# Optimization experiments

Hardware: AMD Instinct MI355X
Metric: run time of the kernel (lower is better)

## Reference

```python
import jax, jax.numpy as jnp
import numpy as np

D_MODEL, HIDDEN, N_EXPERTS, TOP_K = 1024, 2048, 8, 2
RMS_EPS = 1e-6


def setup_inputs() -> dict:
    key = jax.random.key(0)
    ks = jax.random.split(key, 6)
    B, S = 4, 2048
    return {
        "x": jax.random.normal(ks[0], (B, S, D_MODEL), jnp.float32),
        "norm_weight": jnp.ones((D_MODEL,), jnp.float32),
        "gate_w": jax.random.normal(ks[1], (N_EXPERTS, D_MODEL), jnp.float32) * 0.02,
        "w1": jax.random.normal(ks[2], (N_EXPERTS, HIDDEN, D_MODEL), jnp.float32) * 0.02,
        "b1": jnp.zeros((N_EXPERTS, HIDDEN), jnp.float32),
        "w2": jax.random.normal(ks[3], (N_EXPERTS, D_MODEL, HIDDEN), jnp.float32) * 0.02,
        "b2": jnp.zeros((N_EXPERTS, D_MODEL), jnp.float32),
    }


def reference(x, norm_weight, gate_w, w1, b1, w2, b2):
    B, S, D = x.shape
    E = gate_w.shape[0]
    # RMSNorm
    t = x * jax.lax.rsqrt(jnp.mean(x * x, axis=-1, keepdims=True) + RMS_EPS) * norm_weight
    tokens = t.reshape(-1, D)                      # [T, D]
    T = tokens.shape[0]
    # Top-k routing (eval mode: no gate noise)
    gate_logits = tokens @ gate_w.T                # [T, E]
    gate_scores, expert_idx = jax.lax.top_k(gate_logits, TOP_K)
    routing_weights = jax.nn.softmax(gate_scores, axis=-1)  # [T, K]
    # Per-token per-expert combine weight (scatter routing weights into [T, E])
    combine = jnp.zeros((T, E), tokens.dtype).at[
        jnp.arange(T)[:, None], expert_idx
    ].add(routing_weights)
    # Scan over experts; inactive tokens have combine weight 0, matching the
    # masked gather/scatter-add math of the original exactly.
    def body(acc, params):
        W1, B1, W2, B2, c = params                 # c: [T]
        h = jax.nn.gelu(tokens @ W1.T + B1, approximate=False)  # [T, H]
        o = h @ W2.T + B2                          # [T, D]
        return acc + c[:, None] * o, None

    out, _ = jax.lax.scan(body, jnp.zeros_like(tokens), (w1, b1, w2, b2, combine.T))
    return x + out.reshape(B, S, D)
```

## Files before the change

kernel.cpp:

```cpp
#include <hip/hip_runtime.h>
#include <hip/hip_bf16.h>
#include <stdint.h>

#define D_MODEL 1024
#define HIDDEN  2048
#define N_EXP   8
#define T_TOK   8192
#define MAXPOS  17408
#define ROWTILES (MAXPOS/128)

typedef __attribute__((ext_vector_type(4))) float f32x4;
typedef __attribute__((ext_vector_type(8))) short short8v;

__device__ __forceinline__ unsigned short f2bf(float f) {
    union { float f; unsigned int u; } v; v.f = f;
    unsigned int u = v.u;
    unsigned int r = (u + 0x7fffu + ((u >> 16) & 1u)) >> 16;
    return (unsigned short)r;
}

__device__ __forceinline__ void gload_lds16(const void* g, void* l) {
    __builtin_amdgcn_global_load_lds(
        reinterpret_cast<const __attribute__((address_space(1))) unsigned int*>(
            reinterpret_cast<uintptr_t>(g)),
        reinterpret_cast<__attribute__((address_space(3))) unsigned int*>(
            (uint32_t)reinterpret_cast<uintptr_t>(l)),
        16, 0, 0);
}

__global__ void rms_gate_kernel(const float* __restrict__ x,
                                const float* __restrict__ nw,
                                const float* __restrict__ gw,
                                unsigned short* __restrict__ tb,
                                int* __restrict__ tok_e,
                                float* __restrict__ tok_w) {
    const int wave = threadIdx.x >> 6;
    const int lane = threadIdx.x & 63;
    const int t = blockIdx.x * 4 + wave;

    const float4* xr = (const float4*)(x + (size_t)t * D_MODEL);
    const float4* wr = (const float4*)nw;
    float4 xv[4], wv[4];
    #pragma unroll
    for (int j = 0; j < 4; j++) {
        xv[j] = xr[j * 64 + lane];
        wv[j] = wr[j * 64 + lane];
    }

    float ssq = 0.0f;
    #pragma unroll
    for (int j = 0; j < 4; j++)
        ssq += xv[j].x * xv[j].x + xv[j].y * xv[j].y + xv[j].z * xv[j].z + xv[j].w * xv[j].w;
    #pragma unroll
    for (int off = 32; off; off >>= 1) ssq += __shfl_xor(ssq, off);
    const float scale = rsqrtf(ssq * (1.0f / D_MODEL) + 1e-6f);

    float4 tn[4];
    #pragma unroll
    for (int j = 0; j < 4; j++) {
        tn[j].x = xv[j].x * wv[j].x * scale;
        tn[j].y = xv[j].y * wv[j].y * scale;
        tn[j].z = xv[j].z * wv[j].z * scale;
        tn[j].w = xv[j].w * wv[j].w * scale;
    }

    ushort4* tw = (ushort4*)(tb + (size_t)t * D_MODEL);
    #pragma unroll
    for (int j = 0; j < 4; j++) {
        ushort4 o;
        o.x = f2bf(tn[j].x); o.y = f2bf(tn[j].y);
        o.z = f2bf(tn[j].z); o.w = f2bf(tn[j].w);
        tw[j * 64 + lane] = o;
    }

    float d[8];
    #pragma unroll
    for (int e = 0; e < 8; e++) {
        d[e] = 0.0f;
        #pragma unroll
        for (int j = 0; j < 4; j++) {
            float4 g = ((const float4*)(gw + e * D_MODEL))[j * 64 + lane];
            d[e] += tn[j].x * g.x + tn[j].y * g.y + tn[j].z * g.z + tn[j].w * g.w;
        }
    }
    #pragma unroll
    for (int e = 0; e < 8; e++) {
        #pragma unroll
        for (int off = 32; off; off >>= 1) d[e] += __shfl_xor(d[e], off);
    }

    if (lane == 0) {
        int i0 = 0;
        #pragma unroll
        for (int e = 1; e < 8; e++) if (d[e] > d[i0]) i0 = e;
        int i1 = -1;
        #pragma unroll
        for (int e = 0; e < 8; e++)
            if (e != i0 && (i1 < 0 || d[e] > d[i1])) i1 = e;
        float e1 = expf(d[i1] - d[i0]);
        float w0 = 1.0f / (1.0f + e1);
        ((int2*)tok_e)[t]   = make_int2(i0, i1);
        ((float2*)tok_w)[t] = make_float2(w0, e1 * w0);
    }
}

__global__ void hist_kernel(const int* __restrict__ tok_e, int* __restrict__ counts) {
    __shared__ int lh[8];
    if (threadIdx.x < 8) lh[threadIdx.x] = 0;
    __syncthreads();
    int i = blockIdx.x * 512 + threadIdx.x;
    atomicAdd(&lh[tok_e[i]], 1);
    atomicAdd(&lh[tok_e[i + 256]], 1);
    __syncthreads();
    if (threadIdx.x < 8) atomicAdd(&counts[threadIdx.x], lh[threadIdx.x]);
}

__global__ void scan_fill_kernel(int* __restrict__ perm_tok, float* __restrict__ perm_w,
                                 const int* __restrict__ counts,
                                 int* __restrict__ poff, int* __restrict__ pos_ctr) {
    int i = blockIdx.x * 256 + threadIdx.x;
    if (i < MAXPOS) { perm_tok[i] = 0; perm_w[i] = 0.0f; }
    if (blockIdx.x == 0 && threadIdx.x == 0) {
        int acc = 0; poff[0] = 0;
        #pragma unroll
        for (int e = 0; e < 8; e++) {
            pos_ctr[e] = 0;
            acc += (counts[e] + 127) & ~127;
            poff[e + 1] = acc;
        }
    }
}

__global__ void scatter_kernel(const int* __restrict__ tok_e, const float* __restrict__ tok_w,
                               const int* __restrict__ poff, int* __restrict__ pos_ctr,
                               int* __restrict__ perm_tok, float* __restrict__ perm_w) {
    __shared__ int lh[8], lbase[8];
    if (threadIdx.x < 8) lh[threadIdx.x] = 0;
    __syncthreads();
    int t = blockIdx.x * 256 + threadIdx.x;
    int2   ee = ((const int2*)tok_e)[t];
    float2 ww = ((const float2*)tok_w)[t];
    int p0 = atomicAdd(&lh[ee.x], 1);
    int p1 = atomicAdd(&lh[ee.y], 1);
    __syncthreads();
    if (threadIdx.x < 8) lbase[threadIdx.x] = atomicAdd(&pos_ctr[threadIdx.x], lh[threadIdx.x]);
    __syncthreads();
    int q0 = poff[ee.x] + lbase[ee.x] + p0;
    int q1 = poff[ee.y] + lbase[ee.y] + p1;
    perm_tok[q0] = t; perm_w[q0] = ww.x;
    perm_tok[q1] = t; perm_w[q1] = ww.y;
}

__global__ void cvt_bf16_kernel(const float4* __restrict__ in,
                                ushort4* __restrict__ outp, int n4) {
    int i = blockIdx.x * blockDim.x + threadIdx.x;
    if (i >= n4) return;
    float4 v = in[i];
    ushort4 o; o.x = f2bf(v.x); o.y = f2bf(v.y); o.z = f2bf(v.z); o.w = f2bf(v.w);
    outp[i] = o;
}

template <int MODE, int K, int N>
__global__ void moe_gemm_kernel(const unsigned short* __restrict__ A,
                                const unsigned short* __restrict__ W,
                                const float* __restrict__ bias,
                                const int* __restrict__ perm_tok,
                                const float* __restrict__ perm_w,
                                const int* __restrict__ poff,
                                unsigned short* __restrict__ Hout,
                                float* __restrict__ Out) {
    constexpr int NT = N / 128;
    __shared__ short lds[2 * 128 * 64];
    short* Asm = lds;
    short* Bsm = lds + 128 * 64;

    const int nwg = gridDim.x;
    const int cpx = nwg >> 3;
    const int bid = (int)blockIdx.x;
    const int swz = (bid & 7) * cpx + (bid >> 3);

    const int rt = swz / NT, nt = swz % NT;
    const int row_base = rt * 128;
    if (row_base >= poff[8]) return;
    int e = 0;
    while (poff[e + 1] <= row_base) ++e;
    const int n0 = nt * 128;

    const int tid = threadIdx.x;
    const int wave = tid >> 6, lane = tid & 63;
    const int colb = (tid & 7) * 16;
    const int wr = wave >> 1, wc = wave & 1;

    size_t aoff[4], boff[4];
    #pragma unroll
    for (int i = 0; i < 4; i++) {
        int r = row_base + i * 32 + (tid >> 3);
        int arow = (MODE == 1) ? perm_tok[r] : r;
        aoff[i] = (size_t)arow * (K * 2);
        int brow = n0 + i * 32 + (tid >> 3);
        boff[i] = ((size_t)e * N + brow) * (size_t)(K * 2);
    }
    const char* Ab = (const char*)A;
    const char* Wb = (const char*)W;

    f32x4 acc[4][4];
    #pragma unroll
    for (int mi = 0; mi < 4; mi++)
        #pragma unroll
        for (int ni = 0; ni < 4; ni++) acc[mi][ni] = (f32x4)(0.0f);

    for (int k0b = 0; k0b < K * 2; k0b += 128) {
        #pragma unroll
        for (int i = 0; i < 4; i++) {
            gload_lds16(Ab + aoff[i] + k0b + colb, (char*)Asm + i * 4096 + wave * 1024);
            gload_lds16(Wb + boff[i] + k0b + colb, (char*)Bsm + i * 4096 + wave * 1024);
        }
        __syncthreads();
        #pragma unroll
        for (int kk = 0; kk < 2; kk++) {
            short8v af[4], bf[4];
            #pragma unroll
            for (int mi = 0; mi < 4; mi++)
                af[mi] = *(const short8v*)&Asm[(wr * 64 + mi * 16 + (lane & 15)) * 64 + kk * 32 + (lane >> 4) * 8];
            #pragma unroll
            for (int ni = 0; ni < 4; ni++)
                bf[ni] = *(const short8v*)&Bsm[(wc * 64 + ni * 16 + (lane & 15)) * 64 + kk * 32 + (lane >> 4) * 8];
            #pragma unroll
            for (int mi = 0; mi < 4; mi++)
                #pragma unroll
                for (int ni = 0; ni < 4; ni++)
                    acc[mi][ni] = __builtin_amdgcn_mfma_f32_16x16x32_bf16(af[mi], bf[ni], acc[mi][ni], 0, 0, 0);
        }
        __syncthreads();
    }

    if (MODE == 1) {
        #pragma unroll
        for (int mi = 0; mi < 4; mi++) {
            #pragma unroll
            for (int ni = 0; ni < 4; ni++) {
                int c = n0 + wc * 64 + ni * 16 + (lane & 15);
                float bv = bias[e * N + c];
                #pragma unroll
                for (int j = 0; j < 4; j++) {
                    int r = row_base + wr * 64 + mi * 16 + (lane >> 4) * 4 + j;
                    float v = acc[mi][ni][j] + bv;
                    v = 0.5f * v * (1.0f + erff(v * 0.70710678118654752f));
                    Hout[(size_t)r * N + c] = f2bf(v);
                }
            }
        }
    } else {
        #pragma unroll
        for (int mi = 0; mi < 4; mi++) {
            #pragma unroll
            for (int j = 0; j < 4; j++) {
                int r = row_base + wr * 64 + mi * 16 + (lane >> 4) * 4 + j;
                float wgt = perm_w[r];
                if (wgt != 0.0f) {
                    int tok = perm_tok[r];
                    float* orow = Out + (size_t)tok * N;
                    #pragma unroll
                    for (int ni = 0; ni < 4; ni++) {
                        int c = n0 + wc * 64 + ni * 16 + (lane & 15);
                        atomicAdd(&orow[c], wgt * (acc[mi][ni][j] + bias[e * N + c]));
                    }
                }
            }
        }
    }
}

extern "C" void kernel_launch(void* const* d_in, const int* in_sizes, int n_in,
                              void* d_out, int out_size, void* d_ws, size_t ws_size,
                              hipStream_t stream) {
    const float* x  = (const float*)d_in[0];
    const float* nw = (const float*)d_in[1];
    const float* gw = (const float*)d_in[2];
    const float* w1 = (const float*)d_in[3];
    const float* b1 = (const float*)d_in[4];
    const float* w2 = (const float*)d_in[5];
    const float* b2 = (const float*)d_in[6];
    float* out = (float*)d_out;
    char* ws = (char*)d_ws;

    size_t off = 0;
    unsigned short* tb  = (unsigned short*)(ws + off); off += (size_t)T_TOK * D_MODEL * 2;
    unsigned short* w1b = (unsigned short*)(ws + off); off += (size_t)N_EXP * HIDDEN * D_MODEL * 2;
    unsigned short* w2b = (unsigned short*)(ws + off); off += (size_t)N_EXP * D_MODEL * HIDDEN * 2;
    unsigned short* h   = (unsigned short*)(ws + off); off += (size_t)MAXPOS * HIDDEN * 2;
    int*   perm_tok = (int*)(ws + off);   off += MAXPOS * 4;
    float* perm_w   = (float*)(ws + off); off += MAXPOS * 4;
    int*   tok_e    = (int*)(ws + off);   off += T_TOK * 2 * 4;
    float* tok_w    = (float*)(ws + off); off += T_TOK * 2 * 4;
    int*   meta     = (int*)(ws + off);
    int* counts  = meta;
    int* pos_ctr = meta + 8;
    int* poff    = meta + 16;

    hipMemsetAsync(meta, 0, 32, stream);
    hipMemcpyAsync(out, x, (size_t)T_TOK * D_MODEL * 4,
                   hipMemcpyDeviceToDevice, stream);

    rms_gate_kernel<<<T_TOK / 4, 256, 0, stream>>>(x, nw, gw, tb, tok_e, tok_w);

    const int n4 = N_EXP * HIDDEN * D_MODEL / 4;
    cvt_bf16_kernel<<<n4 / 256, 256, 0, stream>>>((const float4*)w1, (ushort4*)w1b, n4);
    cvt_bf16_kernel<<<n4 / 256, 256, 0, stream>>>((const float4*)w2, (ushort4*)w2b, n4);

    hist_kernel<<<32, 256, 0, stream>>>(tok_e, counts);
    scan_fill_kernel<<<MAXPOS / 256, 256, 0, stream>>>(perm_tok, perm_w, counts, poff, pos_ctr);
    scatter_kernel<<<T_TOK / 256, 256, 0, stream>>>(tok_e, tok_w, poff, pos_ctr, perm_tok, perm_w);

    moe_gemm_kernel<1, D_MODEL, HIDDEN><<<ROWTILES * (HIDDEN / 128), 256, 0, stream>>>(
        tb, w1b, b1, perm_tok, perm_w, poff, h, nullptr);
    moe_gemm_kernel<2, HIDDEN, D_MODEL><<<ROWTILES * (D_MODEL / 128), 256, 0, stream>>>(
        h, w2b, b2, perm_tok, perm_w, poff, nullptr, out);
}
```

Measured before the change: 356.9 us.

## Replace atomic scatter-add with bf16 expert output buffer and gather combine kernel

The second expert GEMM no longer scatters weighted fp32 atomicAdds into the output. It writes its bias-added result as bf16 into a permuted buffer, staging it through padded LDS so the global stores are coalesced. A new combine kernel gathers each token's two expert rows, applies the routing weights and adds the residual, which also replaces the device-to-device copy of x into the output. The goal is to remove atomic traffic and the extra copy. In exchange it adds a bf16 rounding of the expert output and an extra intermediate buffer pass.

```diff
diff --git a/kernel.cpp b/kernel.cpp
--- a/kernel.cpp
+++ b/kernel.cpp
@@ -17,6 +17,10 @@
     unsigned int u = v.u;
     unsigned int r = (u + 0x7fffu + ((u >> 16) & 1u)) >> 16;
     return (unsigned short)r;
+}
+__device__ __forceinline__ float bf2f(unsigned short s) {
+    union { unsigned int u; float f; } v; v.u = ((unsigned int)s) << 16;
+    return v.f;
 }
 
 __device__ __forceinline__ void gload_lds16(const void* g, void* l) {
@@ -115,11 +119,11 @@
     if (threadIdx.x < 8) atomicAdd(&counts[threadIdx.x], lh[threadIdx.x]);
 }
 
-__global__ void scan_fill_kernel(int* __restrict__ perm_tok, float* __restrict__ perm_w,
+__global__ void scan_fill_kernel(int* __restrict__ perm_tok,
                                  const int* __restrict__ counts,
                                  int* __restrict__ poff, int* __restrict__ pos_ctr) {
     int i = blockIdx.x * 256 + threadIdx.x;
-    if (i < MAXPOS) { perm_tok[i] = 0; perm_w[i] = 0.0f; }
+    if (i < MAXPOS) perm_tok[i] = 0;
     if (blockIdx.x == 0 && threadIdx.x == 0) {
         int acc = 0; poff[0] = 0;
         #pragma unroll
@@ -131,15 +135,14 @@
     }
 }
 
-__global__ void scatter_kernel(const int* __restrict__ tok_e, const float* __restrict__ tok_w,
+__global__ void scatter_kernel(const int* __restrict__ tok_e,
                                const int* __restrict__ poff, int* __restrict__ pos_ctr,
-                               int* __restrict__ perm_tok, float* __restrict__ perm_w) {
+                               int* __restrict__ perm_tok, int* __restrict__ tok_pos) {
     __shared__ int lh[8], lbase[8];
     if (threadIdx.x < 8) lh[threadIdx.x] = 0;
     __syncthreads();
     int t = blockIdx.x * 256 + threadIdx.x;
-    int2   ee = ((const int2*)tok_e)[t];
-    float2 ww = ((const float2*)tok_w)[t];
+    int2 ee = ((const int2*)tok_e)[t];
     int p0 = atomicAdd(&lh[ee.x], 1);
     int p1 = atomicAdd(&lh[ee.y], 1);
     __syncthreads();
@@ -147,8 +150,9 @@
     __syncthreads();
     int q0 = poff[ee.x] + lbase[ee.x] + p0;
     int q1 = poff[ee.y] + lbase[ee.y] + p1;
-    perm_tok[q0] = t; perm_w[q0] = ww.x;
-    perm_tok[q1] = t; perm_w[q1] = ww.y;
+    perm_tok[q0] = t;
+    perm_tok[q1] = t;
+    ((int2*)tok_pos)[t] = make_int2(q0, q1);
 }
 
 __global__ void cvt_bf16_kernel(const float4* __restrict__ in,
@@ -161,18 +165,17 @@
 }
 
 template <int MODE, int K, int N>
-__global__ void moe_gemm_kernel(const unsigned short* __restrict__ A,
+__global__ __launch_bounds__(256) void moe_gemm_kernel(
+                                const unsigned short* __restrict__ A,
                                 const unsigned short* __restrict__ W,
                                 const float* __restrict__ bias,
                                 const int* __restrict__ perm_tok,
-                                const float* __restrict__ perm_w,
                                 const int* __restrict__ poff,
-                                unsigned short* __restrict__ Hout,
-                                float* __restrict__ Out) {
+                                unsigned short* __restrict__ Cout) {
     constexpr int NT = N / 128;
-    __shared__ short lds[2 * 128 * 64];
+    __shared__ short lds[17408];
     short* Asm = lds;
-    short* Bsm = lds + 128 * 64;
+    short* Bsm = lds + 8192;
 
     const int nwg = gridDim.x;
     const int cpx = nwg >> 3;
@@ -234,40 +237,61 @@
         __syncthreads();
     }
 
-    if (MODE == 1) {
-        #pragma unroll
-        for (int mi = 0; mi < 4; mi++) {
-            #pragma unroll
-            for (int ni = 0; ni < 4; ni++) {
-                int c = n0 + wc * 64 + ni * 16 + (lane & 15);
-                float bv = bias[e * N + c];
-                #pragma unroll
-                for (int j = 0; j < 4; j++) {
-                    int r = row_base + wr * 64 + mi * 16 + (lane >> 4) * 4 + j;
-                    float v = acc[mi][ni][j] + bv;
-                    v = 0.5f * v * (1.0f + erff(v * 0.70710678118654752f));
-                    Hout[(size_t)r * N + c] = f2bf(v);
-                }
-            }
-        }
-    } else {
-        #pragma unroll
-        for (int mi = 0; mi < 4; mi++) {
+    #pragma unroll
+    for (int mi = 0; mi < 4; mi++) {
+        #pragma unroll
+        for (int ni = 0; ni < 4; ni++) {
+            int lc = wc * 64 + ni * 16 + (lane & 15);
+            float bv = bias[e * N + n0 + lc];
             #pragma unroll
             for (int j = 0; j < 4; j++) {
-                int r = row_base + wr * 64 + mi * 16 + (lane >> 4) * 4 + j;
-                float wgt = perm_w[r];
-                if (wgt != 0.0f) {
-                    int tok = perm_tok[r];
-                    float* orow = Out + (size_t)tok * N;
-                    #pragma unroll
-                    for (int ni = 0; ni < 4; ni++) {
-                        int c = n0 + wc * 64 + ni * 16 + (lane & 15);
-                        atomicAdd(&orow[c], wgt * (acc[mi][ni][j] + bias[e * N + c]));
-                    }
-                }
+                int lr = wr * 64 + mi * 16 + (lane >> 4) * 4 + j;
+                float v = acc[mi][ni][j] + bv;
+                if (MODE == 1)
+                    v = 0.5f * v * (1.0f + erff(v * 0.70710678118654752f));
+                lds[lr * 136 + lc] = (short)f2bf(v);
             }
         }
+    }
+    __syncthreads();
+    {
+        const int rr = tid >> 4;
+        const int cc = tid & 15;
+        #pragma unroll
+        for (int p = 0; p < 8; p++) {
+            int lr = p * 16 + rr;
+            short8v vv = *(const short8v*)&lds[lr * 136 + cc * 8];
+            *(short8v*)(Cout + (size_t)(row_base + lr) * N + n0 + cc * 8) = vv;
+        }
+    }
+}
+
+__global__ void combine_kernel(const float* __restrict__ x,
+                               const int* __restrict__ tok_pos,
+                               const float* __restrict__ tok_w,
+                               const unsigned short* __restrict__ obuf,
+                               float* __restrict__ out) {
+    const int wave = threadIdx.x >> 6;
+    const int lane = threadIdx.x & 63;
+    const int t = blockIdx.x * 4 + wave;
+    int2 pp = ((const int2*)tok_pos)[t];
+    float2 ww = ((const float2*)tok_w)[t];
+    const float4* xr = (const float4*)(x + (size_t)t * D_MODEL);
+    float4* orow = (float4*)(out + (size_t)t * D_MODEL);
+    const short4* o0 = (const short4*)(obuf + (size_t)pp.x * D_MODEL);
+    const short4* o1 = (const short4*)(obuf + (size_t)pp.y * D_MODEL);
+    #pragma unroll
+    for (int j = 0; j < 4; j++) {
+        int idx = j * 64 + lane;
+        float4 xv = xr[idx];
+        short4 a = o0[idx];
+        short4 b = o1[idx];
+        float4 r;
+        r.x = xv.x + ww.x * bf2f((unsigned short)a.x) + ww.y * bf2f((unsigned short)b.x);
+        r.y = xv.y + ww.x * bf2f((unsigned short)a.y) + ww.y * bf2f((unsigned short)b.y);
+        r.z = xv.z + ww.x * bf2f((unsigned short)a.z) + ww.y * bf2f((unsigned short)b.z);
+        r.w = xv.w + ww.x * bf2f((unsigned short)a.w) + ww.y * bf2f((unsigned short)b.w);
+        orow[idx] = r;
     }
 }
 
@@ -285,22 +309,21 @@
     char* ws = (char*)d_ws;
 
     size_t off = 0;
-    unsigned short* tb  = (unsigned short*)(ws + off); off += (size_t)T_TOK * D_MODEL * 2;
-    unsigned short* w1b = (unsigned short*)(ws + off); off += (size_t)N_EXP * HIDDEN * D_MODEL * 2;
-    unsigned short* w2b = (unsigned short*)(ws + off); off += (size_t)N_EXP * D_MODEL * HIDDEN * 2;
-    unsigned short* h   = (unsigned short*)(ws + off); off += (size_t)MAXPOS * HIDDEN * 2;
+    unsigned short* tb   = (unsigned short*)(ws + off); off += (size_t)T_TOK * D_MODEL * 2;
+    unsigned short* w1b  = (unsigned short*)(ws + off); off += (size_t)N_EXP * HIDDEN * D_MODEL * 2;
+    unsigned short* w2b  = (unsigned short*)(ws + off); off += (size_t)N_EXP * D_MODEL * HIDDEN * 2;
+    unsigned short* h    = (unsigned short*)(ws + off); off += (size_t)MAXPOS * HIDDEN * 2;
+    unsigned short* obuf = (unsigned short*)(ws + off); off += (size_t)MAXPOS * D_MODEL * 2;
     int*   perm_tok = (int*)(ws + off);   off += MAXPOS * 4;
-    float* perm_w   = (float*)(ws + off); off += MAXPOS * 4;
     int*   tok_e    = (int*)(ws + off);   off += T_TOK * 2 * 4;
     float* tok_w    = (float*)(ws + off); off += T_TOK * 2 * 4;
+    int*   tok_pos  = (int*)(ws + off);   off += T_TOK * 2 * 4;
     int*   meta     = (int*)(ws + off);
     int* counts  = meta;
     int* pos_ctr = meta + 8;
     int* poff    = meta + 16;
 
     hipMemsetAsync(meta, 0, 32, stream);
-    hipMemcpyAsync(out, x, (size_t)T_TOK * D_MODEL * 4,
-                   hipMemcpyDeviceToDevice, stream);
 
     rms_gate_kernel<<<T_TOK / 4, 256, 0, stream>>>(x, nw, gw, tb, tok_e, tok_w);
 
@@ -309,11 +332,13 @@
     cvt_bf16_kernel<<<n4 / 256, 256, 0, stream>>>((const float4*)w2, (ushort4*)w2b, n4);
 
     hist_kernel<<<32, 256, 0, stream>>>(tok_e, counts);
-    scan_fill_kernel<<<MAXPOS / 256, 256, 0, stream>>>(perm_tok, perm_w, counts, poff, pos_ctr);
-    scatter_kernel<<<T_TOK / 256, 256, 0, stream>>>(tok_e, tok_w, poff, pos_ctr, perm_tok, perm_w);
+    scan_fill_kernel<<<MAXPOS / 256, 256, 0, stream>>>(perm_tok, counts, poff, pos_ctr);
+    scatter_kernel<<<T_TOK / 256, 256, 0, stream>>>(tok_e, poff, pos_ctr, perm_tok, tok_pos);
 
     moe_gemm_kernel<1, D_MODEL, HIDDEN><<<ROWTILES * (HIDDEN / 128), 256, 0, stream>>>(
-        tb, w1b, b1, perm_tok, perm_w, poff, h, nullptr);
+        tb, w1b, b1, perm_tok, poff, h);
     moe_gemm_kernel<2, HIDDEN, D_MODEL><<<ROWTILES * (D_MODEL / 128), 256, 0, stream>>>(
-        h, w2b, b2, perm_tok, perm_w, poff, nullptr, out);
-}
+        h, w2b, b2, perm_tok, poff, obuf);
+
+    combine_kernel<<<T_TOK / 4, 256, 0, stream>>>(x, tok_pos, tok_w, obuf, out);
+}
```

New measurement: 384.9 us. +7.8%, slower.
